# Performance work log

Measured on AMD Instinct MI355X. Metric: run time of the kernel, lower is better.

## Reference

```python
import jax, jax.numpy as jnp
import numpy as np

M = 512          # feature_dim
NH = 8           # num_heads
FFN = 2048       # ffn_hidden_dim
NMOD = 4         # modalities (seq len for attention)
EPS = 1e-5


def setup_inputs() -> dict:
    key = jax.random.key(0)
    ks = jax.random.split(key, 16)
    B, H = 64, 256
    s = 0.02
    return {
        "x_image": jax.random.normal(ks[0], (B, H, M), jnp.float32),
        "x_radar": jax.random.normal(ks[1], (B, H, M), jnp.float32),
        "x_lidar": jax.random.normal(ks[2], (B, H, M), jnp.float32),
        "x_gps":   jax.random.normal(ks[3], (B, H, M), jnp.float32),
        # nn.MultiheadAttention params (torch layout: weight is (out,in))
        "in_proj_w": jax.random.normal(ks[4], (3 * M, M), jnp.float32) * s,
        "in_proj_b": jnp.zeros((3 * M,), jnp.float32),
        "out_proj_w": jax.random.normal(ks[5], (M, M), jnp.float32) * s,
        "out_proj_b": jnp.zeros((M,), jnp.float32),
        "ln1_g": jnp.ones((M,), jnp.float32),
        "ln1_b": jnp.zeros((M,), jnp.float32),
        "w1": jax.random.normal(ks[6], (FFN, M), jnp.float32) * s,
        "b1": jnp.zeros((FFN,), jnp.float32),
        "w2": jax.random.normal(ks[7], (M, FFN), jnp.float32) * s,
        "b2": jnp.zeros((M,), jnp.float32),
        "ln2_g": jnp.ones((M,), jnp.float32),
        "ln2_b": jnpp if False else jnp.zeros((M,), jnp.float32),
    }


def _layernorm(x, g, b):
    mu = jnp.mean(x, axis=-1, keepdims=True)
    var = jnp.mean((x - mu) ** 2, axis=-1, keepdims=True)
    return (x - mu) * jax.lax.rsqrt(var + EPS) * g + b


def _forward(x_image, x_radar, x_lidar, x_gps,
             in_proj_w, in_proj_b, out_proj_w, out_proj_b,
             ln1_g, ln1_b, w1, b1, w2, b2, ln2_g, ln2_b):
    B, H, _ = x_image.shape
    # F: (B*H, NMOD, M) -- fold batch and time; per-t loop is independent
    F = jnp.stack([x_image, x_radar, x_lidar, x_gps], axis=2).reshape(B * H, NMOD, M)
    qkv = F @ in_proj_w.T + in_proj_b              # (N, NMOD, 3M)
    q, k, v = jnp.split(qkv, 3, axis=-1)
    dh = M // NH
    def heads(t):  # (N, NMOD, M) -> (N, NH, NMOD, dh)
        return t.reshape(-1, NMOD, NH, dh).transpose(0, 2, 1, 3)
    qh, kh, vh = heads(q), heads(k), heads(v)
    scores = jnp.einsum("bhsd,bhtd->bhst", qh, kh) / np.sqrt(dh).astype(np.float32)
    attn = jax.nn.softmax(scores, axis=-1)
    o = jnp.einsum("bhst,bhtd->bhsd", attn, vh)
    o = o.transpose(0, 2, 1, 3).reshape(-1, NMOD, M)
    attn_out = o @ out_proj_w.T + out_proj_b
    h1 = _layernorm(F + attn_out, ln1_g, ln1_b)    # (N, NMOD, M)
    agg = h1.sum(axis=1)                            # (N, M)
    ffn = jax.nn.gelu(agg @ w1.T + b1, approximate=False) @ w2.T + b2
    z = _layernorm(agg + ffn, ln2_g, ln2_b)
    return z.reshape(B, H, M)


def reference(x_image, x_radar, x_lidar, x_gps,
              in_proj_w, in_proj_b, out_proj_w, out_proj_b,
              ln1_g, ln1_b, w1, b1, w2, b2, ln2_g, ln2_b):
    return _forward(x_image, x_radar, x_lidar, x_gps,
                    in_proj_w, in_proj_b, out_proj_w, out_proj_b,
                    ln1_g, ln1_b, w1, b1, w2, b2, ln2_g, ln2_b)
```

## Files before the change

### kernel.cpp

```cpp
#include <hip/hip_runtime.h>
#include <hip/hip_bf16.h>


typedef __attribute__((ext_vector_type(8))) short s16x8;
typedef __attribute__((ext_vector_type(4))) float f32x4;

__device__ __forceinline__ unsigned short f2bf(float f) {
  unsigned int u = __float_as_uint(f);
  u += 0x7fffu + ((u >> 16) & 1u);
  return (unsigned short)(u >> 16);
}
__device__ __forceinline__ float bf2f(unsigned short s) {
  return __uint_as_float(((unsigned int)s) << 16);
}
__device__ __forceinline__ f32x4 mfma16(s16x8 a, s16x8 b, f32x4 c) {
  return __builtin_amdgcn_mfma_f32_16x16x32_bf16(a, b, c, 0, 0, 0);
}
__device__ __forceinline__ int swz(int row, int bir) {
  return row * 128 + ((((row) & 7) << 4) ^ bir);
}
__device__ __forceinline__ int qkswz(int row, int c) {
  return row * 128 + ((((c >> 3) ^ (row & 7)) << 4)) + (c & 7) * 2;
}
__device__ __forceinline__ int vtswz(int d, int row) {
  return d * 256 + ((((row >> 3) ^ (d & 7)) << 4)) + (row & 7) * 2;
}
__device__ __forceinline__ int pwswz(int row, int c) {
  return row * 64 + ((((c >> 3) ^ (row & 3)) << 4)) + (c & 7) * 2;
}
__device__ __forceinline__ int vtoff(int r, int c) {
  return r * 1024 + ((c * 2) ^ ((r & 7) << 4));
}
__device__ __forceinline__ void gl_lds16(const void* g, void* l) {
  __builtin_amdgcn_global_load_lds(
      (const __attribute__((address_space(1))) unsigned int*)g,
      (__attribute__((address_space(3))) unsigned int*)l, 16, 0, 0);
}

__global__ void pack_kernel(const float* __restrict__ wqkv, const float* __restrict__ wout,
                            const float* __restrict__ w1, const float* __restrict__ w2,
                            const float* __restrict__ x0, const float* __restrict__ x1,
                            const float* __restrict__ x2, const float* __restrict__ x3,
                            unsigned short* __restrict__ o_wqkv, unsigned short* __restrict__ o_wout,
                            unsigned short* __restrict__ o_w1, unsigned short* __restrict__ o_w2,
                            unsigned short* __restrict__ o_x4) {
  const long c0 = 196608, c1 = 262144, c2 = 524288, c3 = 786432, c4 = 9175040;
  for (long v = (long)blockIdx.x * blockDim.x + threadIdx.x; v < c4;
       v += (long)gridDim.x * blockDim.x) {
    const float* src;
    unsigned short* dst;
    if (v < c0) { src = wqkv + v * 4; dst = o_wqkv + v * 4; }
    else if (v < c1) { long u = v - c0; src = wout + u * 4; dst = o_wout + u * 4; }
    else if (v < c2) { long u = v - c1; src = w1 + u * 4; dst = o_w1 + u * 4; }
    else if (v < c3) { long u = v - c2; src = w2 + u * 4; dst = o_w2 + u * 4; }
    else {
      long u = v - c3; long e = u * 4; long r = e >> 9; int i = (int)(e & 511);
      int s = (int)(r & 3); long n = r >> 2;
      const float* xs = (s == 0) ? x0 : (s == 1) ? x1 : (s == 2) ? x2 : x3;
      src = xs + n * 512 + i; dst = o_x4 + e;
    }
    float4 f = *reinterpret_cast<const float4*>(src);
    ushort4 hb;
    hb.x = f2bf(f.x); hb.y = f2bf(f.y); hb.z = f2bf(f.z); hb.w = f2bf(f.w);
    *reinterpret_cast<ushort4*>(dst) = hb;
  }
}

__launch_bounds__(256, 2)
__global__ void qkv_attn_kernel(const unsigned short* __restrict__ x4,
                                const unsigned short* __restrict__ wqkv,
                                const float* __restrict__ in_b,
                                unsigned short* __restrict__ o_out) {
  const int wg = blockIdx.x;
  const int slot = wg >> 3, xcd = wg & 7;
  const int tb = ((slot >> 3) << 3) | xcd;
  const int h = slot & 7;
  const int tid = threadIdx.x, lane = tid & 63, w = tid >> 6;
  const int wm = w >> 1, wn = w & 1;

  __shared__ __align__(16) unsigned char smem[49152];
  unsigned short* aT = (unsigned short*)smem;
  unsigned short* bT = (unsigned short*)(smem + 16384);
  unsigned short* Qs = (unsigned short*)smem;
  unsigned short* Ks = (unsigned short*)(smem + 16384);
  unsigned short* Vt = (unsigned short*)(smem + 32768);
  unsigned short* Pw = (unsigned short*)smem;
  unsigned short* outT = (unsigned short*)(smem + 16384);

  f32x4 acc[4][6];
#pragma unroll
  for (int i = 0; i < 4; ++i)
#pragma unroll
    for (int j = 0; j < 6; ++j) acc[i][j] = (f32x4){0.f, 0.f, 0.f, 0.f};

  const long rowBase = (long)tb * 128;
  const int loff = ((lane >> 3) * 512) + (((lane & 7) ^ (lane >> 3)) * 8);

  for (int kk = 0; kk < 8; ++kk) {
    const int k0 = kk * 64;
#pragma unroll
    for (int it = 0; it < 4; ++it) {
      int c = w * 4 + it;
      gl_lds16(x4 + (rowBase + c * 8) * 512 + k0 + loff, aT + c * 512);
    }
#pragma unroll
    for (int it = 0; it < 6; ++it) {
      int c = w * 6 + it;
      int bc0 = c * 8;
      int wb = (bc0 < 64) ? (h * 64 + bc0)
             : (bc0 < 128) ? (512 + h * 64 + (bc0 - 64))
                           : (1024 + h * 64 + (bc0 - 128));
      gl_lds16(wqkv + (long)wb * 512 + k0 + loff, bT + c * 512);
    }
    __syncthreads();
#pragma unroll
    for (int k2 = 0; k2 < 2; ++k2) {
      s16x8 af[4], bfr[6];
      const int bir = k2 * 64 + ((lane >> 4) << 4);
#pragma unroll
      for (int mi = 0; mi < 4; ++mi) {
        int row = wm * 64 + mi * 16 + (lane & 15);
        af[mi] = *(const s16x8*)((unsigned char*)aT + swz(row, bir));
      }
#pragma unroll
      for (int ni = 0; ni < 6; ++ni) {
        int col = wn * 96 + ni * 16 + (lane & 15);
        bfr[ni] = *(const s16x8*)((unsigned char*)bT + swz(col, bir));
      }
#pragma unroll
      for (int mi = 0; mi < 4; ++mi)
#pragma unroll
        for (int ni = 0; ni < 6; ++ni)
          acc[mi][ni] = mfma16(af[mi], bfr[ni], acc[mi][ni]);
    }
    __syncthreads();
  }

#pragma unroll
  for (int mi = 0; mi < 4; ++mi)
#pragma unroll
    for (int ni = 0; ni < 6; ++ni) {
      int col = wn * 96 + ni * 16 + (lane & 15);
      int wb = (col < 64) ? (h * 64 + col)
             : (col < 128) ? (512 + h * 64 + (col - 64))
                           : (1024 + h * 64 + (col - 128));
      float bias = in_b[wb];
      int row0 = wm * 64 + mi * 16 + ((lane >> 4) << 2);
#pragma unroll
      for (int r = 0; r < 4; ++r) {
        int row = row0 + r;
        unsigned short hv = f2bf(acc[mi][ni][r] + bias);
        if (col < 64)
          *(unsigned short*)((unsigned char*)Qs + qkswz(row, col)) = hv;
        else if (col < 128)
          *(unsigned short*)((unsigned char*)Ks + qkswz(row, col - 64)) = hv;
        else
          *(unsigned short*)((unsigned char*)Vt + vtswz(col - 128, row)) = hv;
      }
    }
  __syncthreads();

  f32x4 sacc[2];
#pragma unroll
  for (int i2 = 0; i2 < 2; ++i2) {
    int ti = w * 2 + i2;
    int qrow = ti * 16 + (lane & 15);
    int bir = (lane >> 4) << 4;
    s16x8 qa0 = *(const s16x8*)((unsigned char*)Qs + swz(qrow, bir));
    s16x8 qa1 = *(const s16x8*)((unsigned char*)Qs + swz(qrow, 64 + bir));
    s16x8 ka0 = *(const s16x8*)((unsigned char*)Ks + swz(qrow, bir));
    s16x8 ka1 = *(const s16x8*)((unsigned char*)Ks + swz(qrow, 64 + bir));
    f32x4 s = (f32x4){0.f, 0.f, 0.f, 0.f};
    s = mfma16(qa0, ka0, s);
    s = mfma16(qa1, ka1, s);
    sacc[i2] = s;
  }
  __syncthreads();
  {
    s16x8 z = (s16x8){0, 0, 0, 0, 0, 0, 0, 0};
    ((s16x8*)Pw)[tid] = z;
    ((s16x8*)Pw)[tid + 256] = z;
  }
  __syncthreads();

  const bool rel = ((lane & 15) >> 2) == (lane >> 4);
#pragma unroll
  for (int i2 = 0; i2 < 2; ++i2) {
    int ti = w * 2 + i2;
#pragma unroll
    for (int r = 0; r < 4; ++r) {
      float sc = sacc[i2][r] * 0.125f;
      float m = fmaxf(sc, __shfl_xor(sc, 1));
      m = fmaxf(m, __shfl_xor(m, 2));
      float e = __expf(sc - m);
      float su = e + __shfl_xor(e, 1);
      su = su + __shfl_xor(su, 2);
      float p = e / su;
      if (rel) {
        int row = ti * 16 + ((lane >> 4) << 2) + r;
        int cl = (((row >> 2) & 7) << 2) + (lane & 3);
        *(unsigned short*)((unsigned char*)Pw + pwswz(row, cl)) = f2bf(p);
      }
    }
  }
  __syncthreads();

#pragma unroll
  for (int i2 = 0; i2 < 2; ++i2) {
    int ti = w * 2 + i2;
    int arow = ti * 16 + (lane & 15);
    s16x8 pa = *(const s16x8*)((unsigned char*)Pw + arow * 64 +
                               ((((lane >> 4) ^ (arow & 3)) << 4)));
    f32x4 pv4[4];
#pragma unroll
    for (int n = 0; n < 4; ++n) {
      int d = n * 16 + (lane & 15);
      int gran = ((ti >> 1) << 2) + (lane >> 4);
      s16x8 vb = *(const s16x8*)((unsigned char*)Vt + d * 256 +
                                 (((gran ^ (d & 7)) << 4)));
      pv4[n] = mfma16(pa, vb, (f32x4){0.f, 0.f, 0.f, 0.f});
    }
#pragma unroll
    for (int n = 0; n < 4; ++n) {
      int d = n * 16 + (lane & 15);
      int row0 = ti * 16 + ((lane >> 4) << 2);
#pragma unroll
      for (int r = 0; r < 4; ++r)
        *(unsigned short*)((unsigned char*)outT + qkswz(row0 + r, d)) =
            f2bf(pv4[n][r]);
    }
  }
  __syncthreads();
#pragma unroll
  for (int j = 0; j < 4; ++j) {
    int c = j * 256 + tid;
    int row = c >> 3, ch = c & 7;
    s16x8 v = *(const s16x8*)((unsigned char*)outT + qkswz(row, ch * 8));
    *(s16x8*)(o_out + (rowBase + row) * 512 + h * 64 + ch * 8) = v;
  }
}

__launch_bounds__(256)
__global__ void outproj_ln1_kernel(const unsigned short* __restrict__ o_in,
                                   const unsigned short* __restrict__ wout,
                                   const float* __restrict__ out_b,
                                   const unsigned short* __restrict__ x4,
                                   const float* __restrict__ ln1_g, const float* __restrict__ ln1_b,
                                   float* __restrict__ agg_f, unsigned short* __restrict__ agg_b) {
  const int tb = blockIdx.x;
  const int tid = threadIdx.x, lane = tid & 63, w = tid >> 6;
  __shared__ __align__(16) unsigned char smem[53504];
  unsigned short* vt = (unsigned short*)smem;
  unsigned short* aT = (unsigned short*)(smem + 32768);
  unsigned short* bT = (unsigned short*)(smem + 36864);
  float* stats = (float*)(smem + 53248);
  const long rowBase = (long)tb * 32;

  for (int ns = 0; ns < 4; ++ns) {
    f32x4 acc[2][2];
#pragma unroll
    for (int i = 0; i < 2; ++i)
#pragma unroll
      for (int j = 0; j < 2; ++j) acc[i][j] = (f32x4){0.f, 0.f, 0.f, 0.f};
    for (int kk = 0; kk < 8; ++kk) {
      const int k0 = kk * 64;
      {
        int lr = tid >> 3, c8 = tid & 7;
        s16x8 v = *(const s16x8*)(o_in + (rowBase + lr) * 512 + k0 + c8 * 8);
        *(s16x8*)((unsigned char*)aT + swz(lr, c8 * 16)) = v;
      }
#pragma unroll
      for (int it = 0; it < 4; ++it) {
        int cid = tid + it * 256, bc = cid >> 3, c8 = cid & 7;
        s16x8 v = *(const s16x8*)(wout + (long)(ns * 128 + bc) * 512 + k0 + c8 * 8);
        *(s16x8*)((unsigned char*)bT + swz(bc, c8 * 16)) = v;
      }
      __syncthreads();
#pragma unroll
      for (int k2 = 0; k2 < 2; ++k2) {
        s16x8 af[2], bfr[2];
        const int bir = k2 * 64 + ((lane >> 4) << 4);
#pragma unroll
        for (int mi = 0; mi < 2; ++mi) {
          int row = mi * 16 + (lane & 15);
          af[mi] = *(const s16x8*)((unsigned char*)aT + swz(row, bir));
        }
#pragma unroll
        for (int ni = 0; ni < 2; ++ni) {
          int col = w * 32 + ni * 16 + (lane & 15);
          bfr[ni] = *(const s16x8*)((unsigned char*)bT + swz(col, bir));
        }
#pragma unroll
        for (int mi = 0; mi < 2; ++mi)
#pragma unroll
          for (int ni = 0; ni < 2; ++ni)
            acc[mi][ni] = mfma16(af[mi], bfr[ni], acc[mi][ni]);
      }
      __syncthreads();
    }
#pragma unroll
    for (int mi = 0; mi < 2; ++mi)
#pragma unroll
      for (int ni = 0; ni < 2; ++ni) {
        int gcol = ns * 128 + w * 32 + ni * 16 + (lane & 15);
        float bias = out_b[gcol];
        int row0 = mi * 16 + ((lane >> 4) << 2);
#pragma unroll
        for (int r = 0; r < 4; ++r) {
          int rr = row0 + r;
          float F = bf2f(x4[(rowBase + rr) * 512 + gcol]);
          *(unsigned short*)((unsigned char*)vt + vtoff(rr, gcol)) =
              f2bf(acc[mi][ni][r] + bias + F);
        }
      }
  }
  __syncthreads();
  {
    int wv = tid >> 6, ln = tid & 63;
    for (int i = 0; i < 8; ++i) {
      int r = wv * 8 + i;
      s16x8 v8 = *(const s16x8*)((unsigned char*)vt + vtoff(r, ln * 8));
      float sum = 0.f, sq = 0.f;
#pragma unroll
      for (int d = 0; d < 8; ++d) {
        float v = bf2f((unsigned short)v8[d]);
        sum += v; sq += v * v;
      }
#pragma unroll
      for (int off = 1; off < 64; off <<= 1) {
        sum += __shfl_xor(sum, off); sq += __shfl_xor(sq, off);
      }
      if (ln == 0) {
        float mu = sum * (1.f / 512.f);
        float var = sq * (1.f / 512.f) - mu * mu;
        stats[r * 2] = mu;
        stats[r * 2 + 1] = rsqrtf(var + 1e-5f);
      }
    }
  }
  __syncthreads();
  for (int it = 0; it < 2; ++it) {
    int ci = tid + it * 256;
    int tok = ci >> 6, c0 = (ci & 63) * 8;
    long gtok = (long)tb * 8 + tok;
    float a[8] = {0.f, 0.f, 0.f, 0.f, 0.f, 0.f, 0.f, 0.f};
#pragma unroll
    for (int s = 0; s < 4; ++s) {
      int r = tok * 4 + s;
      s16x8 v8 = *(const s16x8*)((unsigned char*)vt + vtoff(r, c0));
      float mu = stats[r * 2], is = stats[r * 2 + 1];
#pragma unroll
      for (int d = 0; d < 8; ++d) a[d] += (bf2f((unsigned short)v8[d]) - mu) * is;
    }
    float4 g0 = *(const float4*)(ln1_g + c0);
    float4 g1 = *(const float4*)(ln1_g + c0 + 4);
    float4 b0 = *(const float4*)(ln1_b + c0);
    float4 b1 = *(const float4*)(ln1_b + c0 + 4);
    float ov[8];
    ov[0] = g0.x * a[0] + 4.f * b0.x; ov[1] = g0.y * a[1] + 4.f * b0.y;
    ov[2] = g0.z * a[2] + 4.f * b0.z; ov[3] = g0.w * a[3] + 4.f * b0.w;
    ov[4] = g1.x * a[4] + 4.f * b1.x; ov[5] = g1.y * a[5] + 4.f * b1.y;
    ov[6] = g1.z * a[6] + 4.f * b1.z; ov[7] = g1.w * a[7] + 4.f * b1.w;
    *(float4*)(agg_f + gtok * 512 + c0) = (float4){ov[0], ov[1], ov[2], ov[3]};
    *(float4*)(agg_f + gtok * 512 + c0 + 4) = (float4){ov[4], ov[5], ov[6], ov[7]};
    s16x8 ab;
#pragma unroll
    for (int d = 0; d < 8; ++d) ab[d] = (short)f2bf(ov[d]);
    *(s16x8*)(agg_b + gtok * 512 + c0) = ab;
  }
}

__launch_bounds__(256)
__global__ void ffn1_kernel(const unsigned short* __restrict__ aggb,
                            const unsigned short* __restrict__ w1b,
                            const float* __restrict__ b1,
                            unsigned short* __restrict__ hidden) {
  const int wg = blockIdx.x;
  const int slot = wg >> 3, xcd = wg & 7;
  const int by = ((slot >> 4) << 3) | xcd;
  const int bx = slot & 15;
  const int tid = threadIdx.x, lane = tid & 63, w = tid >> 6;
  const int wm = w >> 1, wn = w & 1;
  __shared__ __align__(16) unsigned char smem[32768];
  unsigned short* aT = (unsigned short*)smem;
  unsigned short* bT = (unsigned short*)(smem + 16384);
  f32x4 acc[4][4];
#pragma unroll
  for (int i = 0; i < 4; ++i)
#pragma unroll
    for (int j = 0; j < 4; ++j) acc[i][j] = (f32x4){0.f, 0.f, 0.f, 0.f};
  const long rowBase = (long)by * 128;
  const long colBase = (long)bx * 128;
  const int loff = ((lane >> 3) * 512) + (((lane & 7) ^ (lane >> 3)) * 8);
  for (int kk = 0; kk < 8; ++kk) {
    const int k0 = kk * 64;
#pragma unroll
    for (int it = 0; it < 4; ++it) {
      int c = w * 4 + it;
      gl_lds16(aggb + (rowBase + c * 8) * 512 + k0 + loff, aT + c * 512);
    }
#pragma unroll
    for (int it = 0; it < 4; ++it) {
      int c = w * 4 + it;
      gl_lds16(w1b + (colBase + c * 8) * 512 + k0 + loff, bT + c * 512);
    }
    __syncthreads();
#pragma unroll
    for (int k2 = 0; k2 < 2; ++k2) {
      s16x8 af[4], bfr[4];
      const int bir = k2 * 64 + ((lane >> 4) << 4);
#pragma unroll
      for (int mi = 0; mi < 4; ++mi) {
        int row = wm * 64 + mi * 16 + (lane & 15);
        af[mi] = *(const s16x8*)((unsigned char*)aT + swz(row, bir));
      }
#pragma unroll
      for (int ni = 0; ni < 4; ++ni) {
        int col = wn * 64 + ni * 16 + (lane & 15);
        bfr[ni] = *(const s16x8*)((unsigned char*)bT + swz(col, bir));
      }
#pragma unroll
      for (int mi = 0; mi < 4; ++mi)
#pragma unroll
        for (int ni = 0; ni < 4; ++ni)
          acc[mi][ni] = mfma16(af[mi], bfr[ni], acc[mi][ni]);
    }
    __syncthreads();
  }
#pragma unroll
  for (int mi = 0; mi < 4; ++mi)
#pragma unroll
    for (int ni = 0; ni < 4; ++ni) {
      long gcol = colBase + wn * 64 + ni * 16 + (lane & 15);
      float bias = b1[gcol];
      int row0 = wm * 64 + mi * 16 + ((lane >> 4) << 2);
#pragma unroll
      for (int r = 0; r < 4; ++r) {
        float x = acc[mi][ni][r] + bias;
        float g = 0.5f * x * (1.f + erff(x * 0.70710678118f));
        hidden[(rowBase + row0 + r) * 2048 + gcol] = f2bf(g);
      }
    }
}

__launch_bounds__(256)
__global__ void ffn2_kernel(const unsigned short* __restrict__ hidden,
                            const unsigned short* __restrict__ w2b,
                            const float* __restrict__ b2,
                            const float* __restrict__ agg_f,
                            float* __restrict__ ffn2s) {
  const int wg = blockIdx.x;
  const int slot = wg >> 3, xcd = wg & 7;
  const int by = ((slot >> 2) << 3) | xcd;
  const int bx = slot & 3;
  const int tid = threadIdx.x, lane = tid & 63, w = tid >> 6;
  const int wm = w >> 1, wn = w & 1;
  __shared__ __align__(16) unsigned char smem[32768];
  unsigned short* aT = (unsigned short*)smem;
  unsigned short* bT = (unsigned short*)(smem + 16384);
  f32x4 acc[4][4];
#pragma unroll
  for (int i = 0; i < 4; ++i)
#pragma unroll
    for (int j = 0; j < 4; ++j) acc[i][j] = (f32x4){0.f, 0.f, 0.f, 0.f};
  const long rowBase = (long)by * 128;
  const long colBase = (long)bx * 128;
  const int loff2k = ((lane >> 3) * 2048) + (((lane & 7) ^ (lane >> 3)) * 8);
  for (int kk = 0; kk < 32; ++kk) {
    const int k0 = kk * 64;
#pragma unroll
    for (int it = 0; it < 4; ++it) {
      int c = w * 4 + it;
      gl_lds16(hidden + (rowBase + c * 8) * 2048 + k0 + loff2k, aT + c * 512);
    }
#pragma unroll
    for (int it = 0; it < 4; ++it) {
      int c = w * 4 + it;
      gl_lds16(w2b + (colBase + c * 8) * 2048 + k0 + loff2k, bT + c * 512);
    }
    __syncthreads();
#pragma unroll
    for (int k2 = 0; k2 < 2; ++k2) {
      s16x8 af[4], bfr[4];
      const int bir = k2 * 64 + ((lane >> 4) << 4);
#pragma unroll
      for (int mi = 0; mi < 4; ++mi) {
        int row = wm * 64 + mi * 16 + (lane & 15);
        af[mi] = *(const s16x8*)((unsigned char*)aT + swz(row, bir));
      }
#pragma unroll
      for (int ni = 0; ni < 4; ++ni) {
        int col = wn * 64 + ni * 16 + (lane & 15);
        bfr[ni] = *(const s16x8*)((unsigned char*)bT + swz(col, bir));
      }
#pragma unroll
      for (int mi = 0; mi < 4; ++mi)
#pragma unroll
        for (int ni = 0; ni < 4; ++ni)
          acc[mi][ni] = mfma16(af[mi], bfr[ni], acc[mi][ni]);
    }
    __syncthreads();
  }
#pragma unroll
  for (int mi = 0; mi < 4; ++mi)
#pragma unroll
    for (int ni = 0; ni < 4; ++ni) {
      long gcol = colBase + wn * 64 + ni * 16 + (lane & 15);
      float bias = b2[gcol];
      int row0 = wm * 64 + mi * 16 + ((lane >> 4) << 2);
#pragma unroll
      for (int r = 0; r < 4; ++r) {
        long grow = rowBase + row0 + r;
        ffn2s[grow * 512 + gcol] = acc[mi][ni][r] + bias + agg_f[grow * 512 + gcol];
      }
    }
}

__launch_bounds__(256)
__global__ void ln2_kernel(const float* __restrict__ ffn2s,
                           const float* __restrict__ ln2_g,
                           const float* __restrict__ ln2_b,
                           float* __restrict__ out) {
  const int tb = blockIdx.x;
  const int lane = threadIdx.x & 63, wv = threadIdx.x >> 6;
  const int c0 = lane * 8;
  float4 g0 = *(const float4*)(ln2_g + c0);
  float4 g1 = *(const float4*)(ln2_g + c0 + 4);
  float4 b0 = *(const float4*)(ln2_b + c0);
  float4 b1 = *(const float4*)(ln2_b + c0 + 4);
#pragma unroll
  for (int i = 0; i < 4; ++i) {
    long row = (long)tb * 16 + wv * 4 + i;
    const float* src = ffn2s + row * 512 + c0;
    float4 a = *(const float4*)src;
    float4 c = *(const float4*)(src + 4);
    float sum = a.x + a.y + a.z + a.w + c.x + c.y + c.z + c.w;
    float sq = a.x * a.x + a.y * a.y + a.z * a.z + a.w * a.w +
               c.x * c.x + c.y * c.y + c.z * c.z + c.w * c.w;
#pragma unroll
    for (int off = 1; off < 64; off <<= 1) {
      sum += __shfl_xor(sum, off); sq += __shfl_xor(sq, off);
    }
    float mu = sum * (1.f / 512.f);
    float is = rsqrtf(sq * (1.f / 512.f) - mu * mu + 1e-5f);
    float* dst = out + row * 512 + c0;
    *(float4*)dst = (float4){(a.x - mu) * is * g0.x + b0.x, (a.y - mu) * is * g0.y + b0.y,
                             (a.z - mu) * is * g0.z + b0.z, (a.w - mu) * is * g0.w + b0.w};
    *(float4*)(dst + 4) = (float4){(c.x - mu) * is * g1.x + b1.x, (c.y - mu) * is * g1.y + b1.y,
                                   (c.z - mu) * is * g1.z + b1.z, (c.w - mu) * is * g1.w + b1.w};
  }
}

extern "C" void kernel_launch(void* const* d_in, const int* in_sizes, int n_in,
                              void* d_out, int out_size, void* d_ws, size_t ws_size,
                              hipStream_t stream) {
  (void)in_sizes; (void)n_in; (void)out_size;
  const float* x0 = (const float*)d_in[0];
  const float* x1 = (const float*)d_in[1];
  const float* x2 = (const float*)d_in[2];
  const float* x3 = (const float*)d_in[3];
  const float* in_w = (const float*)d_in[4];
  const float* in_b = (const float*)d_in[5];
  const float* out_w = (const float*)d_in[6];
  const float* out_b = (const float*)d_in[7];
  const float* ln1_g = (const float*)d_in[8];
  const float* ln1_b = (const float*)d_in[9];
  const float* w1 = (const float*)d_in[10];
  const float* b1 = (const float*)d_in[11];
  const float* w2 = (const float*)d_in[12];
  const float* b2 = (const float*)d_in[13];
  const float* ln2_g = (const float*)d_in[14];
  const float* ln2_b = (const float*)d_in[15];
  float* out = (float*)d_out;

  unsigned char* ws = (unsigned char*)d_ws;
  if (ws_size < 190840832u) return;
  unsigned short* wqkv_b = (unsigned short*)(ws + 0);
  unsigned short* wout_b = (unsigned short*)(ws + 1572864);
  unsigned short* w1_b = (unsigned short*)(ws + 2097152);
  unsigned short* w2_b = (unsigned short*)(ws + 4194304);
  unsigned short* x4 = (unsigned short*)(ws + 6291456);
  unsigned short* o_buf = (unsigned short*)(ws + 73400320);
  float* agg_f = (float*)(ws + 140509184);
  unsigned short* agg_b = (unsigned short*)(ws + 174063616);
  unsigned short* hidden = o_buf;
  float* ffn2s = (float*)(ws + 6291456);

  pack_kernel<<<2048, 256, 0, stream>>>(in_w, out_w, w1, w2, x0, x1, x2, x3,
                                        wqkv_b, wout_b, w1_b, w2_b, x4);
  qkv_attn_kernel<<<4096, 256, 0, stream>>>(x4, wqkv_b, in_b, o_buf);
  outproj_ln1_kernel<<<2048, 256, 0, stream>>>(o_buf, wout_b, out_b, x4,
                                               ln1_g, ln1_b, agg_f, agg_b);
  ffn1_kernel<<<2048, 256, 0, stream>>>(agg_b, w1_b, b1, hidden);
  ffn2_kernel<<<512, 256, 0, stream>>>(hidden, w2_b, b2, agg_f, ffn2s);
  ln2_kernel<<<1024, 256, 0, stream>>>(ffn2s, ln2_g, ln2_b, out);
}
```

Measured before the change: 395.2 us.

## Split outproj into 128x128-tiled GEMM plus separate LN1 kernel; split-K FFN2

The fused out-projection + LN1 kernel, which used 32-row tiles and re-read the weight four times per block, is replaced by a 128x128-tiled GEMM. That GEMM uses direct global-to-LDS loads and writes the residual sum in place into the bf16 input buffer. A separate kernel then does the per-row LayerNorm and the modality sum. FFN2 is split along K into two halves across twice as many workgroups, to fill the GPU better, and LN2 adds the two partial results. In exchange there is an extra kernel launch, an extra round trip of the h1 tensor through global memory, and an extra fp32 partial buffer to write and read.

```diff
diff --git a/kernel.cpp b/kernel.cpp
--- a/kernel.cpp
+++ b/kernel.cpp
@@ -27,9 +27,6 @@
 }
 __device__ __forceinline__ int pwswz(int row, int c) {
   return row * 64 + ((((c >> 3) ^ (row & 3)) << 4)) + (c & 7) * 2;
-}
-__device__ __forceinline__ int vtoff(int r, int c) {
-  return r * 1024 + ((c * 2) ^ ((r & 7) << 4));
 }
 __device__ __forceinline__ void gl_lds16(const void* g, void* l) {
   __builtin_amdgcn_global_load_lds(
@@ -241,132 +238,126 @@
 }
 
 __launch_bounds__(256)
-__global__ void outproj_ln1_kernel(const unsigned short* __restrict__ o_in,
-                                   const unsigned short* __restrict__ wout,
-                                   const float* __restrict__ out_b,
-                                   const unsigned short* __restrict__ x4,
-                                   const float* __restrict__ ln1_g, const float* __restrict__ ln1_b,
-                                   float* __restrict__ agg_f, unsigned short* __restrict__ agg_b) {
+__global__ void outproj_kernel(const unsigned short* __restrict__ o_in,
+                               const unsigned short* __restrict__ wout,
+                               const float* __restrict__ out_b,
+                               unsigned short* __restrict__ x4h1) {
+  const int wg = blockIdx.x;
+  const int slot = wg >> 3, xcd = wg & 7;
+  const int by = ((slot >> 2) << 3) | xcd;
+  const int bx = slot & 3;
+  const int tid = threadIdx.x, lane = tid & 63, w = tid >> 6;
+  const int wm = w >> 1, wn = w & 1;
+  __shared__ __align__(16) unsigned char smem[32768];
+  unsigned short* aT = (unsigned short*)smem;
+  unsigned short* bT = (unsigned short*)(smem + 16384);
+  f32x4 acc[4][4];
+#pragma unroll
+  for (int i = 0; i < 4; ++i)
+#pragma unroll
+    for (int j = 0; j < 4; ++j) acc[i][j] = (f32x4){0.f, 0.f, 0.f, 0.f};
+  const long rowBase = (long)by * 128;
+  const long colBase = (long)bx * 128;
+  const int loff = ((lane >> 3) * 512) + (((lane & 7) ^ (lane >> 3)) * 8);
+  for (int kk = 0; kk < 8; ++kk) {
+    const int k0 = kk * 64;
+#pragma unroll
+    for (int it = 0; it < 4; ++it) {
+      int c = w * 4 + it;
+      gl_lds16(o_in + (rowBase + c * 8) * 512 + k0 + loff, aT + c * 512);
+    }
+#pragma unroll
+    for (int it = 0; it < 4; ++it) {
+      int c = w * 4 + it;
+      gl_lds16(wout + (colBase + c * 8) * 512 + k0 + loff, bT + c * 512);
+    }
+    __syncthreads();
+#pragma unroll
+    for (int k2 = 0; k2 < 2; ++k2) {
+      s16x8 af[4], bfr[4];
+      const int bir = k2 * 64 + ((lane >> 4) << 4);
+#pragma unroll
+      for (int mi = 0; mi < 4; ++mi) {
+        int row = wm * 64 + mi * 16 + (lane & 15);
+        af[mi] = *(const s16x8*)((unsigned char*)aT + swz(row, bir));
+      }
+#pragma unroll
+      for (int ni = 0; ni < 4; ++ni) {
+        int col = wn * 64 + ni * 16 + (lane & 15);
+        bfr[ni] = *(const s16x8*)((unsigned char*)bT + swz(col, bir));
+      }
+#pragma unroll
+      for (int mi = 0; mi < 4; ++mi)
+#pragma unroll
+        for (int ni = 0; ni < 4; ++ni)
+          acc[mi][ni] = mfma16(af[mi], bfr[ni], acc[mi][ni]);
+    }
+    __syncthreads();
+  }
+#pragma unroll
+  for (int mi = 0; mi < 4; ++mi)
+#pragma unroll
+    for (int ni = 0; ni < 4; ++ni) {
+      long gcol = colBase + wn * 64 + ni * 16 + (lane & 15);
+      float bias = out_b[gcol];
+      int row0 = wm * 64 + mi * 16 + ((lane >> 4) << 2);
+#pragma unroll
+      for (int r = 0; r < 4; ++r) {
+        long grow = rowBase + row0 + r;
+        float F = bf2f(x4h1[grow * 512 + gcol]);
+        x4h1[grow * 512 + gcol] = f2bf(acc[mi][ni][r] + bias + F);
+      }
+    }
+}
+
+__launch_bounds__(256)
+__global__ void ln1_agg_kernel(const unsigned short* __restrict__ h1,
+                               const float* __restrict__ ln1_g,
+                               const float* __restrict__ ln1_b,
+                               float* __restrict__ agg_f,
+                               unsigned short* __restrict__ agg_b) {
   const int tb = blockIdx.x;
-  const int tid = threadIdx.x, lane = tid & 63, w = tid >> 6;
-  __shared__ __align__(16) unsigned char smem[53504];
-  unsigned short* vt = (unsigned short*)smem;
-  unsigned short* aT = (unsigned short*)(smem + 32768);
-  unsigned short* bT = (unsigned short*)(smem + 36864);
-  float* stats = (float*)(smem + 53248);
-  const long rowBase = (long)tb * 32;
-
-  for (int ns = 0; ns < 4; ++ns) {
-    f32x4 acc[2][2];
-#pragma unroll
-    for (int i = 0; i < 2; ++i)
-#pragma unroll
-      for (int j = 0; j < 2; ++j) acc[i][j] = (f32x4){0.f, 0.f, 0.f, 0.f};
-    for (int kk = 0; kk < 8; ++kk) {
-      const int k0 = kk * 64;
-      {
-        int lr = tid >> 3, c8 = tid & 7;
-        s16x8 v = *(const s16x8*)(o_in + (rowBase + lr) * 512 + k0 + c8 * 8);
-        *(s16x8*)((unsigned char*)aT + swz(lr, c8 * 16)) = v;
-      }
-#pragma unroll
-      for (int it = 0; it < 4; ++it) {
-        int cid = tid + it * 256, bc = cid >> 3, c8 = cid & 7;
-        s16x8 v = *(const s16x8*)(wout + (long)(ns * 128 + bc) * 512 + k0 + c8 * 8);
-        *(s16x8*)((unsigned char*)bT + swz(bc, c8 * 16)) = v;
-      }
-      __syncthreads();
-#pragma unroll
-      for (int k2 = 0; k2 < 2; ++k2) {
-        s16x8 af[2], bfr[2];
-        const int bir = k2 * 64 + ((lane >> 4) << 4);
-#pragma unroll
-        for (int mi = 0; mi < 2; ++mi) {
-          int row = mi * 16 + (lane & 15);
-          af[mi] = *(const s16x8*)((unsigned char*)aT + swz(row, bir));
-        }
-#pragma unroll
-        for (int ni = 0; ni < 2; ++ni) {
-          int col = w * 32 + ni * 16 + (lane & 15);
-          bfr[ni] = *(const s16x8*)((unsigned char*)bT + swz(col, bir));
-        }
-#pragma unroll
-        for (int mi = 0; mi < 2; ++mi)
-#pragma unroll
-          for (int ni = 0; ni < 2; ++ni)
-            acc[mi][ni] = mfma16(af[mi], bfr[ni], acc[mi][ni]);
-      }
-      __syncthreads();
-    }
-#pragma unroll
-    for (int mi = 0; mi < 2; ++mi)
-#pragma unroll
-      for (int ni = 0; ni < 2; ++ni) {
-        int gcol = ns * 128 + w * 32 + ni * 16 + (lane & 15);
-        float bias = out_b[gcol];
-        int row0 = mi * 16 + ((lane >> 4) << 2);
-#pragma unroll
-        for (int r = 0; r < 4; ++r) {
-          int rr = row0 + r;
-          float F = bf2f(x4[(rowBase + rr) * 512 + gcol]);
-          *(unsigned short*)((unsigned char*)vt + vtoff(rr, gcol)) =
-              f2bf(acc[mi][ni][r] + bias + F);
-        }
-      }
-  }
-  __syncthreads();
-  {
-    int wv = tid >> 6, ln = tid & 63;
-    for (int i = 0; i < 8; ++i) {
-      int r = wv * 8 + i;
-      s16x8 v8 = *(const s16x8*)((unsigned char*)vt + vtoff(r, ln * 8));
+  const int lane = threadIdx.x & 63, wv = threadIdx.x >> 6;
+  const int c0 = lane * 8;
+  float4 g0 = *(const float4*)(ln1_g + c0);
+  float4 g1 = *(const float4*)(ln1_g + c0 + 4);
+  float4 b0 = *(const float4*)(ln1_b + c0);
+  float4 b1 = *(const float4*)(ln1_b + c0 + 4);
+#pragma unroll
+  for (int i = 0; i < 4; ++i) {
+    long t = (long)tb * 16 + wv * 4 + i;
+    float a[8] = {0.f, 0.f, 0.f, 0.f, 0.f, 0.f, 0.f, 0.f};
+#pragma unroll
+    for (int s = 0; s < 4; ++s) {
+      long row = t * 4 + s;
+      s16x8 v8 = *(const s16x8*)(h1 + row * 512 + c0);
+      float vv[8];
       float sum = 0.f, sq = 0.f;
 #pragma unroll
       for (int d = 0; d < 8; ++d) {
-        float v = bf2f((unsigned short)v8[d]);
-        sum += v; sq += v * v;
+        vv[d] = bf2f((unsigned short)v8[d]);
+        sum += vv[d]; sq += vv[d] * vv[d];
       }
 #pragma unroll
       for (int off = 1; off < 64; off <<= 1) {
         sum += __shfl_xor(sum, off); sq += __shfl_xor(sq, off);
       }
-      if (ln == 0) {
-        float mu = sum * (1.f / 512.f);
-        float var = sq * (1.f / 512.f) - mu * mu;
-        stats[r * 2] = mu;
-        stats[r * 2 + 1] = rsqrtf(var + 1e-5f);
-      }
-    }
-  }
-  __syncthreads();
-  for (int it = 0; it < 2; ++it) {
-    int ci = tid + it * 256;
-    int tok = ci >> 6, c0 = (ci & 63) * 8;
-    long gtok = (long)tb * 8 + tok;
-    float a[8] = {0.f, 0.f, 0.f, 0.f, 0.f, 0.f, 0.f, 0.f};
-#pragma unroll
-    for (int s = 0; s < 4; ++s) {
-      int r = tok * 4 + s;
-      s16x8 v8 = *(const s16x8*)((unsigned char*)vt + vtoff(r, c0));
-      float mu = stats[r * 2], is = stats[r * 2 + 1];
-#pragma unroll
-      for (int d = 0; d < 8; ++d) a[d] += (bf2f((unsigned short)v8[d]) - mu) * is;
-    }
-    float4 g0 = *(const float4*)(ln1_g + c0);
-    float4 g1 = *(const float4*)(ln1_g + c0 + 4);
-    float4 b0 = *(const float4*)(ln1_b + c0);
-    float4 b1 = *(const float4*)(ln1_b + c0 + 4);
+      float mu = sum * (1.f / 512.f);
+      float is = rsqrtf(sq * (1.f / 512.f) - mu * mu + 1e-5f);
+#pragma unroll
+      for (int d = 0; d < 8; ++d) a[d] += (vv[d] - mu) * is;
+    }
     float ov[8];
     ov[0] = g0.x * a[0] + 4.f * b0.x; ov[1] = g0.y * a[1] + 4.f * b0.y;
     ov[2] = g0.z * a[2] + 4.f * b0.z; ov[3] = g0.w * a[3] + 4.f * b0.w;
     ov[4] = g1.x * a[4] + 4.f * b1.x; ov[5] = g1.y * a[5] + 4.f * b1.y;
     ov[6] = g1.z * a[6] + 4.f * b1.z; ov[7] = g1.w * a[7] + 4.f * b1.w;
-    *(float4*)(agg_f + gtok * 512 + c0) = (float4){ov[0], ov[1], ov[2], ov[3]};
-    *(float4*)(agg_f + gtok * 512 + c0 + 4) = (float4){ov[4], ov[5], ov[6], ov[7]};
+    *(float4*)(agg_f + t * 512 + c0) = (float4){ov[0], ov[1], ov[2], ov[3]};
+    *(float4*)(agg_f + t * 512 + c0 + 4) = (float4){ov[4], ov[5], ov[6], ov[7]};
     s16x8 ab;
 #pragma unroll
     for (int d = 0; d < 8; ++d) ab[d] = (short)f2bf(ov[d]);
-    *(s16x8*)(agg_b + gtok * 512 + c0) = ab;
+    *(s16x8*)(agg_b + t * 512 + c0) = ab;
   }
 }
 
@@ -448,11 +439,13 @@
                             const unsigned short* __restrict__ w2b,
                             const float* __restrict__ b2,
                             const float* __restrict__ agg_f,
-                            float* __restrict__ ffn2s) {
+                            float* __restrict__ part0,
+                            float* __restrict__ part1) {
   const int wg = blockIdx.x;
-  const int slot = wg >> 3, xcd = wg & 7;
-  const int by = ((slot >> 2) << 3) | xcd;
-  const int bx = slot & 3;
+  const int xcd = wg & 7, slot = wg >> 3;
+  const int g = slot >> 3, sub = slot & 7;
+  const int by = (g << 3) | xcd;
+  const int bx = sub & 3, ks = sub >> 2;
   const int tid = threadIdx.x, lane = tid & 63, w = tid >> 6;
   const int wm = w >> 1, wn = w & 1;
   __shared__ __align__(16) unsigned char smem[32768];
@@ -465,9 +458,10 @@
     for (int j = 0; j < 4; ++j) acc[i][j] = (f32x4){0.f, 0.f, 0.f, 0.f};
   const long rowBase = (long)by * 128;
   const long colBase = (long)bx * 128;
+  const int kBase = ks * 1024;
   const int loff2k = ((lane >> 3) * 2048) + (((lane & 7) ^ (lane >> 3)) * 8);
-  for (int kk = 0; kk < 32; ++kk) {
-    const int k0 = kk * 64;
+  for (int kk = 0; kk < 16; ++kk) {
+    const int k0 = kBase + kk * 64;
 #pragma unroll
     for (int it = 0; it < 4; ++it) {
       int c = w * 4 + it;
@@ -506,18 +500,28 @@
 #pragma unroll
     for (int ni = 0; ni < 4; ++ni) {
       long gcol = colBase + wn * 64 + ni * 16 + (lane & 15);
-      float bias = b2[gcol];
       int row0 = wm * 64 + mi * 16 + ((lane >> 4) << 2);
-#pragma unroll
-      for (int r = 0; r < 4; ++r) {
-        long grow = rowBase + row0 + r;
-        ffn2s[grow * 512 + gcol] = acc[mi][ni][r] + bias + agg_f[grow * 512 + gcol];
+      if (ks == 0) {
+        float bias = b2[gcol];
+#pragma unroll
+        for (int r = 0; r < 4; ++r) {
+          long grow = rowBase + row0 + r;
+          part0[grow * 512 + gcol] =
+              acc[mi][ni][r] + bias + agg_f[grow * 512 + gcol];
+        }
+      } else {
+#pragma unroll
+        for (int r = 0; r < 4; ++r) {
+          long grow = rowBase + row0 + r;
+          part1[grow * 512 + gcol] = acc[mi][ni][r];
+        }
       }
     }
 }
 
 __launch_bounds__(256)
-__global__ void ln2_kernel(const float* __restrict__ ffn2s,
+__global__ void ln2_kernel(const float* __restrict__ p0,
+                           const float* __restrict__ p1,
                            const float* __restrict__ ln2_g,
                            const float* __restrict__ ln2_b,
                            float* __restrict__ out) {
@@ -531,9 +535,14 @@
 #pragma unroll
   for (int i = 0; i < 4; ++i) {
     long row = (long)tb * 16 + wv * 4 + i;
-    const float* src = ffn2s + row * 512 + c0;
-    float4 a = *(const float4*)src;
-    float4 c = *(const float4*)(src + 4);
+    const float* s0 = p0 + row * 512 + c0;
+    const float* s1 = p1 + row * 512 + c0;
+    float4 a0 = *(const float4*)s0;
+    float4 a1 = *(const float4*)(s0 + 4);
+    float4 e0 = *(const float4*)s1;
+    float4 e1 = *(const float4*)(s1 + 4);
+    float4 a = (float4){a0.x + e0.x, a0.y + e0.y, a0.z + e0.z, a0.w + e0.w};
+    float4 c = (float4){a1.x + e1.x, a1.y + e1.y, a1.z + e1.z, a1.w + e1.w};
     float sum = a.x + a.y + a.z + a.w + c.x + c.y + c.z + c.w;
     float sq = a.x * a.x + a.y * a.y + a.z * a.z + a.w * a.w +
                c.x * c.x + c.y * c.y + c.z * c.z + c.w * c.w;
@@ -584,14 +593,15 @@
   float* agg_f = (float*)(ws + 140509184);
   unsigned short* agg_b = (unsigned short*)(ws + 174063616);
   unsigned short* hidden = o_buf;
-  float* ffn2s = (float*)(ws + 6291456);
+  float* part0 = (float*)(ws + 6291456);
+  float* part1 = (float*)(ws + 39845888);
 
   pack_kernel<<<2048, 256, 0, stream>>>(in_w, out_w, w1, w2, x0, x1, x2, x3,
                                         wqkv_b, wout_b, w1_b, w2_b, x4);
   qkv_attn_kernel<<<4096, 256, 0, stream>>>(x4, wqkv_b, in_b, o_buf);
-  outproj_ln1_kernel<<<2048, 256, 0, stream>>>(o_buf, wout_b, out_b, x4,
-                                               ln1_g, ln1_b, agg_f, agg_b);
+  outproj_kernel<<<2048, 256, 0, stream>>>(o_buf, wout_b, out_b, x4);
+  ln1_agg_kernel<<<1024, 256, 0, stream>>>(x4, ln1_g, ln1_b, agg_f, agg_b);
   ffn1_kernel<<<2048, 256, 0, stream>>>(agg_b, w1_b, b1, hidden);
-  ffn2_kernel<<<512, 256, 0, stream>>>(hidden, w2_b, b2, agg_f, ffn2s);
-  ln2_kernel<<<1024, 256, 0, stream>>>(ffn2s, ln2_g, ln2_b, out);
-}
+  ffn2_kernel<<<1024, 256, 0, stream>>>(hidden, w2_b, b2, agg_f, part0, part1);
+  ln2_kernel<<<1024, 256, 0, stream>>>(part0, part1, ln2_g, ln2_b, out);
+}
```

New measurement: 420.4 us. +6.4%, slower.

## Double-buffer QKV GEMM LDS tiles and drop redundant barriers before softmax

Applied to the files above, without the earlier changes.

Splits the QKV projection's shared-memory staging into two buffers so the next K-slice's global-to-LDS loads are issued while the current slice is consumed by MFMA. This hides load latency behind compute. It also gives P and the output tiles their own LDS regions, so the P zero-fill can move before the scores barrier and two __syncthreads are removed. LDS per block grows from 48KB to 80KB, which may limit occupancy under launch_bounds(256,2).

```diff
diff --git a/kernel.cpp b/kernel.cpp
--- a/kernel.cpp
+++ b/kernel.cpp
@@ -78,14 +78,12 @@
   const int tid = threadIdx.x, lane = tid & 63, w = tid >> 6;
   const int wm = w >> 1, wn = w & 1;
 
-  __shared__ __align__(16) unsigned char smem[49152];
-  unsigned short* aT = (unsigned short*)smem;
-  unsigned short* bT = (unsigned short*)(smem + 16384);
+  __shared__ __align__(16) unsigned char smem[81920];
   unsigned short* Qs = (unsigned short*)smem;
   unsigned short* Ks = (unsigned short*)(smem + 16384);
   unsigned short* Vt = (unsigned short*)(smem + 32768);
-  unsigned short* Pw = (unsigned short*)smem;
-  unsigned short* outT = (unsigned short*)(smem + 16384);
+  unsigned short* Pw = (unsigned short*)(smem + 49152);
+  unsigned short* outT = (unsigned short*)(smem + 57344);
 
   f32x4 acc[4][6];
 #pragma unroll
@@ -96,23 +94,35 @@
   const long rowBase = (long)tb * 128;
   const int loff = ((lane >> 3) * 512) + (((lane & 7) ^ (lane >> 3)) * 8);
 
+#define K1_STAGE(BUF, KK)                                                       \
+  {                                                                             \
+    unsigned short* aT_ = (unsigned short*)(smem + (BUF)*40960);                \
+    unsigned short* bT_ = (unsigned short*)(smem + (BUF)*40960 + 16384);        \
+    const int k0_ = (KK)*64;                                                    \
+    _Pragma("unroll")                                                           \
+    for (int it = 0; it < 4; ++it) {                                            \
+      int c = w * 4 + it;                                                       \
+      gl_lds16(x4 + (rowBase + c * 8) * 512 + k0_ + loff, aT_ + c * 512);       \
+    }                                                                           \
+    _Pragma("unroll")                                                           \
+    for (int it = 0; it < 6; ++it) {                                            \
+      int c = w * 6 + it;                                                       \
+      int bc0 = c * 8;                                                          \
+      int wb = (bc0 < 64) ? (h * 64 + bc0)                                      \
+             : (bc0 < 128) ? (512 + h * 64 + (bc0 - 64))                        \
+                           : (1024 + h * 64 + (bc0 - 128));                     \
+      gl_lds16(wqkv + (long)wb * 512 + k0_ + loff, bT_ + c * 512);              \
+    }                                                                           \
+  }
+
+  K1_STAGE(0, 0);
+  __syncthreads();
+#pragma unroll
   for (int kk = 0; kk < 8; ++kk) {
-    const int k0 = kk * 64;
-#pragma unroll
-    for (int it = 0; it < 4; ++it) {
-      int c = w * 4 + it;
-      gl_lds16(x4 + (rowBase + c * 8) * 512 + k0 + loff, aT + c * 512);
-    }
-#pragma unroll
-    for (int it = 0; it < 6; ++it) {
-      int c = w * 6 + it;
-      int bc0 = c * 8;
-      int wb = (bc0 < 64) ? (h * 64 + bc0)
-             : (bc0 < 128) ? (512 + h * 64 + (bc0 - 64))
-                           : (1024 + h * 64 + (bc0 - 128));
-      gl_lds16(wqkv + (long)wb * 512 + k0 + loff, bT + c * 512);
-    }
-    __syncthreads();
+    const int cur = kk & 1;
+    if (kk < 7) K1_STAGE(cur ^ 1, kk + 1);
+    unsigned short* aT = (unsigned short*)(smem + cur * 40960);
+    unsigned short* bT = (unsigned short*)(smem + cur * 40960 + 16384);
 #pragma unroll
     for (int k2 = 0; k2 < 2; ++k2) {
       s16x8 af[4], bfr[6];
@@ -135,6 +145,7 @@
     }
     __syncthreads();
   }
+#undef K1_STAGE
 
 #pragma unroll
   for (int mi = 0; mi < 4; ++mi)
@@ -158,6 +169,11 @@
           *(unsigned short*)((unsigned char*)Vt + vtswz(col - 128, row)) = hv;
       }
     }
+  {
+    s16x8 z = (s16x8){0, 0, 0, 0, 0, 0, 0, 0};
+    ((s16x8*)Pw)[tid] = z;
+    ((s16x8*)Pw)[tid + 256] = z;
+  }
   __syncthreads();
 
   f32x4 sacc[2];
@@ -175,13 +191,6 @@
     s = mfma16(qa1, ka1, s);
     sacc[i2] = s;
   }
-  __syncthreads();
-  {
-    s16x8 z = (s16x8){0, 0, 0, 0, 0, 0, 0, 0};
-    ((s16x8*)Pw)[tid] = z;
-    ((s16x8*)Pw)[tid + 256] = z;
-  }
-  __syncthreads();
 
   const bool rel = ((lane & 15) >> 2) == (lane >> 4);
 #pragma unroll
```

Measured after the change: 404.9 us. 1.02x slower.
